# Kernel optimization log

Measured on AMD Instinct MI355X. Metric: run time of the kernel, lower is better.

The kernel has to match this reference:

```python
import jax, jax.numpy as jnp
import numpy as np

B = 256          # graphs per batch
N = 128          # nodes per graph (equal-size graphs; batch is block-contiguous)
P = N * (N - 1) // 2  # pairs per graph = 8128
E = B * 1024     # total edges
D = 128          # node feature dim
L = 32           # latent dim

# precomputed local upper-triangular pair indices (constants)
_PI, _PJ = np.triu_indices(N, k=1)
_PI = jnp.asarray(_PI); _PJ = jnp.asarray(_PJ)


def setup_inputs() -> dict:
    key = jax.random.key(0)
    ks = jax.random.split(key, 8)
    x = jax.random.normal(ks[0], (B * N, D), dtype=jnp.float32)
    # within-graph edges with local i < j
    li = jax.random.randint(ks[1], (E,), 0, N - 1)
    r = jax.random.randint(ks[2], (E,), 0, 1 << 30)
    lj = li + 1 + r % (N - 1 - li)
    g = jax.random.randint(ks[3], (E,), 0, B)
    off = g * N
    edge_index = jnp.stack([off + li, off + lj]).astype(jnp.int64)
    batch = jnp.repeat(jnp.arange(B), N).astype(jnp.int64)
    eps = jax.random.normal(ks[4], (B * N, L), dtype=jnp.float32)
    W1 = jax.random.normal(ks[5], (D, D), dtype=jnp.float32) * 0.05
    b1 = jnp.zeros((D,), dtype=jnp.float32)
    Wmu = jax.random.normal(ks[6], (D, L), dtype=jnp.float32) * 0.05
    bmu = jnp.zeros((L,), dtype=jnp.float32)
    Wls = jax.random.normal(ks[7], (D, L), dtype=jnp.float32) * 0.05
    bls = jnp.zeros((L,), dtype=jnp.float32)
    return {"x": x, "edge_index": edge_index, "batch": batch, "eps": eps,
            "W1": W1, "b1": b1, "Wmu": Wmu, "bmu": bmu, "Wls": Wls, "bls": bls}


def reference(x, edge_index, batch, eps, W1, b1, Wmu, bmu, Wls, bls):
    src, dst = edge_index[0], edge_index[1]
    # --- encoder: one symmetric message-passing layer -> Gaussian q per node ---
    agg = jnp.zeros_like(x).at[dst].add(x[src]).at[src].add(x[dst])
    h = jax.nn.relu((x + agg) @ W1 + b1)
    mu = h @ Wmu + bmu                       # [BN, L]
    log_std = h @ Wls + bls
    std = jnp.exp(log_std)
    z = mu + std * eps                       # rsample
    # --- KL(q || N(0,I)) per node, summed per graph (kls[b]) ---
    kl_node = 0.5 * jnp.sum(std * std + mu * mu - 1.0 - 2.0 * log_std, axis=-1)
    kls = jax.ops.segment_sum(kl_node, batch, num_segments=B)  # [B]
    # --- link targets: scatter edges into triangular pair slots ---
    li, lj, be = src % N, dst % N, src // N
    pidx = li * (2 * N - li - 1) // 2 + (lj - li - 1)
    targets = jnp.zeros((B, P), dtype=z.dtype).at[be, pidx].set(1.0)
    # --- inner-product Bernoulli decoder over all pairs of every graph ---
    zb = z.reshape(B, N, L)
    logits = jnp.einsum('bpl,bpl->bp', zb[:, _PI], zb[:, _PJ])   # [B, P]
    log_probs = jnp.sum(targets * logits - jax.nn.softplus(logits), axis=-1)  # [B]
    elbo = jnp.mean(log_probs - kls)
    return -elbo
```

## Files before the change

kernel.cpp:

```cpp
#include <hip/hip_runtime.h>
#include <math.h>

#define B_ 256
#define N_ 128
#define D_ 128
#define L_ 32
#define E_ 262144
#define PW_ 254
#define DCAP 96

#define NDEG_OFF 0
#define BM_OFF   32768
#define KLS_OFF  97792
#define LP_OFF   98048
#define DONE_OFF 98304
#define ADJ_OFF  98320
#define Z_OFF    884752
#define ZERO_WORDS 98320

__global__ __launch_bounds__(256) void k_build(
    const int* __restrict__ ei, unsigned* __restrict__ ndeg,
    unsigned char* __restrict__ adj, unsigned* __restrict__ bm)
{
    int e = blockIdx.x * 256 + threadIdx.x;
    int src = ei[e], dst = ei[E_ + e];
    unsigned s1 = atomicAdd(&ndeg[src], 1u);
    if (s1 < DCAP) adj[(size_t)src * DCAP + s1] = (unsigned char)(dst & 127);
    unsigned s2 = atomicAdd(&ndeg[dst], 1u);
    if (s2 < DCAP) adj[(size_t)dst * DCAP + s2] = (unsigned char)(src & 127);
    int li = src & 127, lj = dst & 127, g = src >> 7;
    int p = li * (255 - li) / 2 + (lj - li - 1);
    atomicOr(&bm[g * PW_ + (p >> 5)], 1u << (p & 31));
}

__global__ __launch_bounds__(256, 6) void k_encoder(
    const float* __restrict__ x, const unsigned* __restrict__ ndeg,
    const unsigned char* __restrict__ adj,
    const float* __restrict__ W1, const float* __restrict__ b1,
    const float* __restrict__ Wmu, const float* __restrict__ bmu,
    const float* __restrict__ Wls, const float* __restrict__ bls,
    const float* __restrict__ eps,
    float* __restrict__ z, float* __restrict__ kls)
{
    __shared__ float XAs[32 * 132];
    int t = threadIdx.x;
    int g = blockIdx.x & 255;
    int quar = blockIdx.x >> 8;
    int row0 = g * 128 + quar * 32;
    int rg = t >> 5;
    int cg = t & 31;
    int lane = t & 63;

    {
        int nidx = t >> 4;
        int fo = (t & 15) * 8;
        for (int p = 0; p < 2; ++p) {
            int lrow = p * 16 + nidx;
            int gnode = row0 + lrow;
            const float* xr = x + (size_t)gnode * 128 + fo;
            float4 a0 = *(const float4*)xr;
            float4 a1 = *(const float4*)(xr + 4);
            int deg = (int)ndeg[gnode];
            if (deg > DCAP) deg = DCAP;
            const unsigned char* al = adj + (size_t)gnode * DCAP;
            const float* gx = x + (size_t)(gnode & ~127) * 128 + fo;
            int e = 0;
            for (; e + 4 <= deg; e += 4) {
                unsigned pk = *(const unsigned*)(al + e);
                const float* r0 = gx + (pk & 255u) * 128;
                const float* r1 = gx + ((pk >> 8) & 255u) * 128;
                const float* r2 = gx + ((pk >> 16) & 255u) * 128;
                const float* r3 = gx + (pk >> 24) * 128;
                float4 v00 = *(const float4*)r0, v01 = *(const float4*)(r0 + 4);
                float4 v10 = *(const float4*)r1, v11 = *(const float4*)(r1 + 4);
                float4 v20 = *(const float4*)r2, v21 = *(const float4*)(r2 + 4);
                float4 v30 = *(const float4*)r3, v31 = *(const float4*)(r3 + 4);
                a0.x += v00.x + v10.x + v20.x + v30.x;
                a0.y += v00.y + v10.y + v20.y + v30.y;
                a0.z += v00.z + v10.z + v20.z + v30.z;
                a0.w += v00.w + v10.w + v20.w + v30.w;
                a1.x += v01.x + v11.x + v21.x + v31.x;
                a1.y += v01.y + v11.y + v21.y + v31.y;
                a1.z += v01.z + v11.z + v21.z + v31.z;
                a1.w += v01.w + v11.w + v21.w + v31.w;
            }
            for (; e < deg; ++e) {
                const float* r = gx + (unsigned)al[e] * 128;
                float4 v0 = *(const float4*)r, v1 = *(const float4*)(r + 4);
                a0.x += v0.x; a0.y += v0.y; a0.z += v0.z; a0.w += v0.w;
                a1.x += v1.x; a1.y += v1.y; a1.z += v1.z; a1.w += v1.w;
            }
            *(float4*)(XAs + lrow * 132 + fo) = a0;
            *(float4*)(XAs + lrow * 132 + fo + 4) = a1;
        }
    }
    __syncthreads();

    float acc[4][4];
    #pragma unroll
    for (int i = 0; i < 4; ++i)
        #pragma unroll
        for (int j = 0; j < 4; ++j) acc[i][j] = 0.f;

    {
        const float* Wp = W1 + 4 * cg;
        #pragma unroll 2
        for (int k = 0; k < 128; k += 4) {
            float4 av[4], wv[4];
            #pragma unroll
            for (int i = 0; i < 4; ++i)
                av[i] = *(const float4*)(XAs + (4 * rg + i) * 132 + k);
            #pragma unroll
            for (int dk = 0; dk < 4; ++dk)
                wv[dk] = *(const float4*)(Wp + (k + dk) * 128);
            #pragma unroll
            for (int i = 0; i < 4; ++i) {
                acc[i][0] += av[i].x * wv[0].x + av[i].y * wv[1].x + av[i].z * wv[2].x + av[i].w * wv[3].x;
                acc[i][1] += av[i].x * wv[0].y + av[i].y * wv[1].y + av[i].z * wv[2].y + av[i].w * wv[3].y;
                acc[i][2] += av[i].x * wv[0].z + av[i].y * wv[1].z + av[i].z * wv[2].z + av[i].w * wv[3].z;
                acc[i][3] += av[i].x * wv[0].w + av[i].y * wv[1].w + av[i].z * wv[2].w + av[i].w * wv[3].w;
            }
        }
    }

    {
        float4 bb = *(const float4*)(b1 + 4 * cg);
        #pragma unroll
        for (int i = 0; i < 4; ++i) {
            float4 h;
            h.x = fmaxf(acc[i][0] + bb.x, 0.f);
            h.y = fmaxf(acc[i][1] + bb.y, 0.f);
            h.z = fmaxf(acc[i][2] + bb.z, 0.f);
            h.w = fmaxf(acc[i][3] + bb.w, 0.f);
            *(float4*)(XAs + (4 * rg + i) * 132 + 4 * cg) = h;
        }
    }
    __syncthreads();

    float a3[4][2];
    #pragma unroll
    for (int i = 0; i < 4; ++i) { a3[i][0] = 0.f; a3[i][1] = 0.f; }

    {
        const float* W2p = (cg < 16) ? (Wmu + 2 * cg) : (Wls + 2 * (cg - 16));
        #pragma unroll 2
        for (int k = 0; k < 128; k += 4) {
            float4 av[4];
            float2 wv[4];
            #pragma unroll
            for (int i = 0; i < 4; ++i)
                av[i] = *(const float4*)(XAs + (4 * rg + i) * 132 + k);
            #pragma unroll
            for (int dk = 0; dk < 4; ++dk)
                wv[dk] = *(const float2*)(W2p + (k + dk) * 32);
            #pragma unroll
            for (int i = 0; i < 4; ++i) {
                a3[i][0] += av[i].x * wv[0].x + av[i].y * wv[1].x + av[i].z * wv[2].x + av[i].w * wv[3].x;
                a3[i][1] += av[i].x * wv[0].y + av[i].y * wv[1].y + av[i].z * wv[2].y + av[i].w * wv[3].y;
            }
        }
    }
    {
        float2 bv = (cg < 16) ? *(const float2*)(bmu + 2 * cg)
                              : *(const float2*)(bls + 2 * cg - 32);
        #pragma unroll
        for (int i = 0; i < 4; ++i) { a3[i][0] += bv.x; a3[i][1] += bv.y; }
    }

    float o3[4][2];
    #pragma unroll
    for (int i = 0; i < 4; ++i) {
        o3[i][0] = __shfl_xor(a3[i][0], 16);
        o3[i][1] = __shfl_xor(a3[i][1], 16);
    }

    float klsum = 0.f;
    if (cg < 16) {
        int lo = cg;
        #pragma unroll
        for (int i = 0; i < 4; ++i) {
            int rowg = row0 + 4 * rg + i;
            float mu0 = a3[i][0], mu1 = a3[i][1];
            float ls0 = o3[i][0], ls1 = o3[i][1];
            float2 ev = *(const float2*)(eps + (size_t)rowg * 32 + 2 * lo);
            float s0 = __expf(ls0), s1 = __expf(ls1);
            float2 zv = make_float2(mu0 + s0 * ev.x, mu1 + s1 * ev.y);
            *(float2*)(z + (size_t)rowg * 32 + 2 * lo) = zv;
            klsum += s0 * s0 + mu0 * mu0 - 1.f - 2.f * ls0
                   + s1 * s1 + mu1 * mu1 - 1.f - 2.f * ls1;
        }
    }
    #pragma unroll
    for (int off = 32; off > 0; off >>= 1) klsum += __shfl_xor(klsum, off);
    if (lane == 0) atomicAdd(&kls[g], 0.5f * klsum);
}

__global__ __launch_bounds__(256) void k_decoder(
    const float* __restrict__ z, const unsigned* __restrict__ bitmap,
    float* __restrict__ logp, const float* __restrict__ kls,
    unsigned* __restrict__ done, float* __restrict__ out)
{
    __shared__ float zT[32 * 132];
    __shared__ unsigned bm[PW_];
    __shared__ unsigned lastflag;
    int b = blockIdx.x & 255, quar = blockIdx.x >> 8, t = threadIdx.x;

    #pragma unroll
    for (int i = 0; i < 4; ++i) {
        int c = t + i * 256;
        int n = c >> 3, l = (c & 7) << 2;
        float4 v = *(const float4*)(z + ((size_t)b * N_ + n) * L_ + l);
        zT[(l + 0) * 132 + n] = v.x;
        zT[(l + 1) * 132 + n] = v.y;
        zT[(l + 2) * 132 + n] = v.z;
        zT[(l + 3) * 132 + n] = v.w;
    }
    if (t < PW_) bm[t] = bitmap[b * PW_ + t];
    __syncthreads();

    int i0 = quar * 32 + ((t >> 5) << 2);
    int j0 = (t & 31) << 2;
    float gacc[4][4];
    #pragma unroll
    for (int a = 0; a < 4; ++a)
        #pragma unroll
        for (int c = 0; c < 4; ++c) gacc[a][c] = 0.f;

    #pragma unroll 4
    for (int l = 0; l < 32; ++l) {
        float4 a0 = *(const float4*)(zT + l * 132 + i0);
        float4 b0 = *(const float4*)(zT + l * 132 + j0);
        float za[4] = {a0.x, a0.y, a0.z, a0.w};
        float zb[4] = {b0.x, b0.y, b0.z, b0.w};
        #pragma unroll
        for (int a = 0; a < 4; ++a)
            #pragma unroll
            for (int c = 0; c < 4; ++c) gacc[a][c] += za[a] * zb[c];
    }

    float sum = 0.f;
    #pragma unroll
    for (int a = 0; a < 4; ++a) {
        int i = i0 + a;
        #pragma unroll
        for (int c = 0; c < 4; ++c) {
            int j = j0 + c;
            if (j > i) {
                float lg = gacc[a][c];
                int p = i * (255 - i) / 2 + (j - i - 1);
                unsigned bit = (bm[p >> 5] >> (p & 31)) & 1u;
                float sp = __logf(1.f + __expf(-fabsf(lg))) + fmaxf(lg, 0.f);
                sum += bit ? (lg - sp) : (-sp);
            }
        }
    }
    #pragma unroll
    for (int off = 32; off > 0; off >>= 1) sum += __shfl_xor(sum, off);
    if ((t & 63) == 0) atomicAdd(&logp[b], sum);

    __syncthreads();
    if (t == 0) {
        unsigned prev = atomicAdd(done, 1u);
        lastflag = (prev == 4u * B_ - 1u) ? 1u : 0u;
    }
    __syncthreads();
    if (lastflag) {
        float v = __hip_atomic_load(&logp[t], __ATOMIC_RELAXED, __HIP_MEMORY_SCOPE_AGENT)
                - __hip_atomic_load(&kls[t],  __ATOMIC_RELAXED, __HIP_MEMORY_SCOPE_AGENT);
        zT[t] = v;
        __syncthreads();
        for (int s = 128; s > 0; s >>= 1) {
            if (t < s) zT[t] += zT[t + s];
            __syncthreads();
        }
        if (t == 0) out[0] = -zT[0] * (1.0f / 256.0f);
    }
}

extern "C" void kernel_launch(void* const* d_in, const int* in_sizes, int n_in,
                              void* d_out, int out_size, void* d_ws, size_t ws_size,
                              hipStream_t stream) {
    const float* x   = (const float*)d_in[0];
    const int*   ei  = (const int*)d_in[1];
    const float* eps = (const float*)d_in[3];
    const float* W1  = (const float*)d_in[4];
    const float* b1  = (const float*)d_in[5];
    const float* Wmu = (const float*)d_in[6];
    const float* bmu = (const float*)d_in[7];
    const float* Wls = (const float*)d_in[8];
    const float* bls = (const float*)d_in[9];

    unsigned* wsw = (unsigned*)d_ws;
    unsigned*      ndeg = wsw + NDEG_OFF;
    unsigned*      bm   = wsw + BM_OFF;
    float*         kls  = (float*)(wsw + KLS_OFF);
    float*         logp = (float*)(wsw + LP_OFF);
    unsigned*      done = wsw + DONE_OFF;
    unsigned char* adj  = (unsigned char*)(wsw + ADJ_OFF);
    float*         z    = (float*)(wsw + Z_OFF);

    hipMemsetAsync(d_ws, 0, ZERO_WORDS * sizeof(unsigned), stream);

    k_build   <<<E_ / 256, 256, 0, stream>>>(ei, ndeg, adj, bm);
    k_encoder <<<1024, 256, 0, stream>>>(x, ndeg, adj, W1, b1, Wmu, bmu,
                                         Wls, bls, eps, z, kls);
    k_decoder <<<4 * B_, 256, 0, stream>>>(z, bm, logp, kls, done, (float*)d_out);
}
```

Measured before the change: 194.3 us.

## Stage encoder weights through double-buffered LDS with register prefetch; scalarize decoder z transpose

The encoder now streams W1 and the combined Wmu/Wls weights through a double-buffered shared-memory tile, using register prefetch so the next chunk loads while the current one is multiplied. The first load is issued before the gather phase. This replaces direct global/L2 reads of the weights inside the GEMM loops. The change adds 16 KB of LDS and one barrier per chunk, and lowers the occupancy hint from 6 to 4 blocks. Separately, the decoder's z transpose switches from float4 loads with strided LDS stores to scalar loads, which avoids LDS bank conflicts but issues more load instructions.

```diff
diff --git a/kernel.cpp b/kernel.cpp
--- a/kernel.cpp
+++ b/kernel.cpp
@@ -33,7 +33,7 @@
     atomicOr(&bm[g * PW_ + (p >> 5)], 1u << (p & 31));
 }
 
-__global__ __launch_bounds__(256, 6) void k_encoder(
+__global__ __launch_bounds__(256, 4) void k_encoder(
     const float* __restrict__ x, const unsigned* __restrict__ ndeg,
     const unsigned char* __restrict__ adj,
     const float* __restrict__ W1, const float* __restrict__ b1,
@@ -43,6 +43,7 @@
     float* __restrict__ z, float* __restrict__ kls)
 {
     __shared__ float XAs[32 * 132];
+    __shared__ float Ws[2][2048];
     int t = threadIdx.x;
     int g = blockIdx.x & 255;
     int quar = blockIdx.x >> 8;
@@ -50,6 +51,33 @@
     int rg = t >> 5;
     int cg = t & 31;
     int lane = t & 63;
+
+    float4 pre0, pre1;
+    auto issueW1 = [&](int s) {
+        const float4* gp = (const float4*)(W1 + s * 2048);
+        pre0 = gp[t];
+        pre1 = gp[t + 256];
+    };
+    auto issueWB = [&](int ch) {
+        {
+            int c5 = t, row = c5 >> 4, col4 = (c5 & 15) << 2;
+            int rowg = ch * 32 + row;
+            pre0 = (col4 < 32) ? *(const float4*)(Wmu + rowg * 32 + col4)
+                               : *(const float4*)(Wls + rowg * 32 + col4 - 32);
+        }
+        {
+            int c5 = t + 256, row = c5 >> 4, col4 = (c5 & 15) << 2;
+            int rowg = ch * 32 + row;
+            pre1 = (col4 < 32) ? *(const float4*)(Wmu + rowg * 32 + col4)
+                               : *(const float4*)(Wls + rowg * 32 + col4 - 32);
+        }
+    };
+    auto commit = [&](int buf) {
+        ((float4*)Ws[buf])[t] = pre0;
+        ((float4*)Ws[buf])[t + 256] = pre1;
+    };
+
+    issueW1(0);
 
     {
         int nidx = t >> 4;
@@ -94,6 +122,9 @@
             *(float4*)(XAs + lrow * 132 + fo + 4) = a1;
         }
     }
+
+    commit(0);
+    issueW1(1);
     __syncthreads();
 
     float acc[4][4];
@@ -102,17 +133,23 @@
         #pragma unroll
         for (int j = 0; j < 4; ++j) acc[i][j] = 0.f;
 
-    {
-        const float* Wp = W1 + 4 * cg;
-        #pragma unroll 2
-        for (int k = 0; k < 128; k += 4) {
+    #pragma unroll
+    for (int c = 0; c < 8; ++c) {
+        if (c) __syncthreads();
+        if (c < 7) commit((c + 1) & 1);
+        if (c < 6)      issueW1(c + 2);
+        else if (c == 6) issueWB(0);
+        else { commit(0); issueWB(1); }
+        const float* Wb = Ws[c & 1];
+        #pragma unroll
+        for (int k = 0; k < 16; k += 4) {
             float4 av[4], wv[4];
             #pragma unroll
             for (int i = 0; i < 4; ++i)
-                av[i] = *(const float4*)(XAs + (4 * rg + i) * 132 + k);
+                av[i] = *(const float4*)(XAs + (4 * rg + i) * 132 + c * 16 + k);
             #pragma unroll
             for (int dk = 0; dk < 4; ++dk)
-                wv[dk] = *(const float4*)(Wp + (k + dk) * 128);
+                wv[dk] = *(const float4*)(Wb + (k + dk) * 128 + 4 * cg);
             #pragma unroll
             for (int i = 0; i < 4; ++i) {
                 acc[i][0] += av[i].x * wv[0].x + av[i].y * wv[1].x + av[i].z * wv[2].x + av[i].w * wv[3].x;
@@ -141,18 +178,22 @@
     #pragma unroll
     for (int i = 0; i < 4; ++i) { a3[i][0] = 0.f; a3[i][1] = 0.f; }
 
-    {
-        const float* W2p = (cg < 16) ? (Wmu + 2 * cg) : (Wls + 2 * (cg - 16));
-        #pragma unroll 2
-        for (int k = 0; k < 128; k += 4) {
+    #pragma unroll
+    for (int c2 = 0; c2 < 4; ++c2) {
+        if (c2) __syncthreads();
+        if (c2 < 3) commit((c2 + 1) & 1);
+        if (c2 < 2) issueWB(2 + c2);
+        const float* Wb = Ws[c2 & 1];
+        #pragma unroll
+        for (int k = 0; k < 32; k += 4) {
             float4 av[4];
             float2 wv[4];
             #pragma unroll
             for (int i = 0; i < 4; ++i)
-                av[i] = *(const float4*)(XAs + (4 * rg + i) * 132 + k);
+                av[i] = *(const float4*)(XAs + (4 * rg + i) * 132 + c2 * 32 + k);
             #pragma unroll
             for (int dk = 0; dk < 4; ++dk)
-                wv[dk] = *(const float2*)(W2p + (k + dk) * 32);
+                wv[dk] = *(const float2*)(Wb + (k + dk) * 64 + 2 * cg);
             #pragma unroll
             for (int i = 0; i < 4; ++i) {
                 a3[i][0] += av[i].x * wv[0].x + av[i].y * wv[1].x + av[i].z * wv[2].x + av[i].w * wv[3].x;
@@ -206,14 +247,10 @@
     int b = blockIdx.x & 255, quar = blockIdx.x >> 8, t = threadIdx.x;
 
     #pragma unroll
-    for (int i = 0; i < 4; ++i) {
+    for (int i = 0; i < 16; ++i) {
         int c = t + i * 256;
-        int n = c >> 3, l = (c & 7) << 2;
-        float4 v = *(const float4*)(z + ((size_t)b * N_ + n) * L_ + l);
-        zT[(l + 0) * 132 + n] = v.x;
-        zT[(l + 1) * 132 + n] = v.y;
-        zT[(l + 2) * 132 + n] = v.z;
-        zT[(l + 3) * 132 + n] = v.w;
+        int n = c >> 5, l = c & 31;
+        zT[l * 132 + n] = z[((size_t)b * N_ + n) * L_ + l];
     }
     if (t < PW_) bm[t] = bitmap[b * PW_ + t];
     __syncthreads();
```

After: 248.2 us. +27.8%, slower.
